# Kernel tuning notes

Measured on AMD Instinct MI355X. Metric: run time of the kernel, lower is better.

The kernel has to match this reference:

```python
import jax, jax.numpy as jnp
import numpy as np

B, N, D, H = 256, 128, 1024, 4096
PR = 0.2
K1 = int(D * (1 - PR))  # 819 channels kept before net1
K2 = int(H * (1 - PR))  # 3276 channels kept before net2


def setup_inputs() -> dict:
    key = jax.random.key(0)
    ks = jax.random.split(key, 5)
    s = 0.02
    return {
        "x": jax.random.normal(ks[0], (B, N, D), jnp.float32),
        "ws1": jax.random.normal(ks[1], (N,), jnp.float32) * s,  # get_scores1 weight [1,N] -> [N]
        "bs1": jnp.zeros((), jnp.float32),
        "W1": jax.random.normal(ks[2], (H, K1), jnp.float32) * s,  # net1 Linear(K1 -> H)
        "b1": jnp.zeros((H,), jnp.float32),
        "ws2": jax.random.normal(ks[3], (N,), jnp.float32) * s,  # get_scores2 weight
        "bs2": jnp.zeros((), jnp.float32),
        "W2": jax.random.normal(ks[4], (D, K2), jnp.float32) * s,  # net2 Linear(K2 -> D)
        "b2": jnp.zeros((D,), jnp.float32),
    }


def _prune(x, w_s, b_s, k):
    # x: [b, n, c]. Original scores each channel c with Linear(num_patches,1)
    # applied over the patch axis after rearrange to [b, c, n]; equivalent einsum here.
    scores = jnp.einsum('bnc,n->bc', x, w_s) + b_s            # [b, c]
    _, idx = jax.lax.top_k(scores, k)                          # top-k channels per sample
    idx = jnp.sort(idx, axis=-1)                               # boolean-mask gather preserves original channel order
    return jnp.take_along_axis(x, idx[:, None, :], axis=2)    # [b, n, k]


def reference(x, ws1, bs1, W1, b1, ws2, bs2, W2, b2):
    x1 = _prune(x, ws1, bs1, K1)                               # [b, n, K1]
    h = jax.nn.relu(jnp.einsum('bnk,hk->bnh', x1, W1) + b1)    # net1 (dropout=0 eval)
    h2 = _prune(h, ws2, bs2, K2)                               # [b, n, K2]
    return jnp.einsum('bnk,dk->bnd', h2, W2) + b2              # net2
```

## Files before the change

kernel.cpp:

```cpp
#include <hip/hip_runtime.h>
#include <cstdint>
#include <cstddef>

#define B_  256
#define N_  128
#define D_  1024
#define H_  4096
#define K1_ 819
#define K2_ 3276
#define K1P 832
#define K2P 3296
#define KT1 (K1P / 32)
#define KT2 (K2P / 32)

typedef __bf16 bf16x8 __attribute__((ext_vector_type(8)));
typedef float floatx4 __attribute__((ext_vector_type(4)));

__device__ __forceinline__ unsigned short f2bf(float f) {
  unsigned u = __float_as_uint(f);
  u += 0x7FFFu + ((u >> 16) & 1u);
  return (unsigned short)(u >> 16);
}
__device__ __forceinline__ float bf2f(unsigned short s) {
  return __uint_as_float(((unsigned)s) << 16);
}

#define GL16(gp, lp) __builtin_amdgcn_global_load_lds( \
    (const __attribute__((address_space(1))) void*)(gp), \
    (__attribute__((address_space(3))) void*)(lp), 16, 0, 0)

__global__ __launch_bounds__(256) void scores1_kernel(const float* __restrict__ x,
                                                      const float* __restrict__ ws1,
                                                      float* __restrict__ scores1) {
  int b = blockIdx.x, t = threadIdx.x;
  __shared__ float w[N_];
  if (t < N_) w[t] = ws1[t];
  __syncthreads();
  const float* xb = x + (size_t)b * N_ * D_;
  double a0 = 0, a1 = 0, a2 = 0, a3 = 0;
  for (int n = 0; n < N_; ++n) {
    double wv = (double)w[n];
    const float* r = xb + (size_t)n * D_ + t;
    a0 += (double)r[0]   * wv;
    a1 += (double)r[256] * wv;
    a2 += (double)r[512] * wv;
    a3 += (double)r[768] * wv;
  }
  float* s = scores1 + (size_t)b * D_ + t;
  s[0]   = (float)a0;
  s[256] = (float)a1;
  s[512] = (float)a2;
  s[768] = (float)a3;
}

__global__ __launch_bounds__(256) void topk_kernel(const float* __restrict__ scores,
                                                   int C, int K,
                                                   int* __restrict__ idx_out) {
  int b = blockIdx.x, t = threadIdx.x;
  __shared__ unsigned keys[4096];
  __shared__ unsigned hist[256];
  __shared__ unsigned sbuf[256];
  __shared__ unsigned s_sel, s_want, s_bgt, s_beq;

  for (int c = t; c < C; c += 256) {
    unsigned u = __float_as_uint(scores[(size_t)b * C + c]);
    keys[c] = u ^ ((u & 0x80000000u) ? 0xFFFFFFFFu : 0x80000000u);
  }
  if (t == 0) { s_want = (unsigned)K; s_bgt = 0u; s_beq = 0u; }
  __syncthreads();

  unsigned prefix = 0;
  for (int shift = 24; shift >= 0; shift -= 8) {
    hist[t] = 0u;
    __syncthreads();
    unsigned mask = (shift == 24) ? 0u : (0xFFFFFFFFu << (shift + 8));
    for (int c = t; c < C; c += 256) {
      unsigned k = keys[c];
      if ((k & mask) == (prefix & mask))
        atomicAdd(&hist[(k >> shift) & 0xFFu], 1u);
    }
    __syncthreads();
    if (t == 0) {
      unsigned want = s_want, cum = 0u, sel = 0u;
      for (int d = 255; d >= 0; --d) {
        cum += hist[d];
        if (cum >= want) { sel = (unsigned)d; s_want = want - (cum - hist[d]); break; }
      }
      s_sel = sel;
    }
    __syncthreads();
    prefix |= (s_sel << shift);
  }
  unsigned kth = prefix;
  unsigned n_eq_keep = s_want;
  __syncthreads();

  int nch = C >> 8;
  for (int ch = 0; ch < nch; ++ch) {
    int c = (ch << 8) + t;
    unsigned k = keys[c];
    unsigned gt = (k > kth) ? 1u : 0u;
    unsigned eq = (k == kth) ? 1u : 0u;
    unsigned val = gt | (eq << 16);
    sbuf[t] = val;
    __syncthreads();
    unsigned incl = val;
    for (int off = 1; off < 256; off <<= 1) {
      unsigned o = (t >= off) ? sbuf[t - off] : 0u;
      __syncthreads();
      incl += o;
      sbuf[t] = incl;
      __syncthreads();
    }
    unsigned excl = incl - val;
    unsigned gt_ex = excl & 0xFFFFu, eq_ex = excl >> 16;
    unsigned base_gt = s_bgt, base_eq = s_beq;
    unsigned eq_before = base_eq + eq_ex;
    bool keep = (gt != 0u) || ((eq != 0u) && (eq_before < n_eq_keep));
    unsigned kept_eq_before = (eq_before < n_eq_keep) ? eq_before : n_eq_keep;
    unsigned pos = base_gt + gt_ex + kept_eq_before;
    if (keep) idx_out[(size_t)b * K + pos] = c;
    __syncthreads();
    if (t == 255) {
      s_bgt = base_gt + (incl & 0xFFFFu);
      s_beq = base_eq + (incl >> 16);
    }
    __syncthreads();
  }
}

__global__ __launch_bounds__(256) void xprep_kernel(const float* __restrict__ x,
                                                    const int* __restrict__ idx1,
                                                    unsigned short* __restrict__ xch,
                                                    unsigned short* __restrict__ xcl) {
  int bn = blockIdx.x;
  int b = bn >> 7;
  const int* idxb = idx1 + (size_t)b * K1_;
  const float* xr = x + (size_t)bn * D_;
  unsigned short* oh = xch + (size_t)bn * K1P;
  unsigned short* ol = xcl + (size_t)bn * K1P;
  for (int j = threadIdx.x; j < K1P; j += 256) {
    float v = (j < K1_) ? xr[idxb[j]] : 0.f;
    unsigned short hi = f2bf(v);
    unsigned short lo = f2bf(v - bf2f(hi));
    oh[j] = hi;
    ol[j] = lo;
  }
}

__global__ __launch_bounds__(256) void w1split_kernel(const float* __restrict__ W1,
                                                      unsigned short* __restrict__ w1h,
                                                      unsigned short* __restrict__ w1l) {
  int e = blockIdx.x * 256 + threadIdx.x;
  int k = e % K1P, row = e / K1P;
  float v = (k < K1_) ? W1[(size_t)row * K1_ + k] : 0.f;
  unsigned short hi = f2bf(v);
  unsigned short lo = f2bf(v - bf2f(hi));
  w1h[e] = hi;
  w1l[e] = lo;
}

__global__ __launch_bounds__(256) void w2conv_kernel(const float* __restrict__ W2,
                                                     unsigned short* __restrict__ w2b) {
  int e = blockIdx.x * 256 + threadIdx.x;
  int k = e % K2P, row = e / K2P;
  w2b[e] = (k < K2_) ? f2bf(W2[(size_t)row * K2_ + k]) : (unsigned short)0;
}

__global__ __launch_bounds__(256) void hcompact_kernel(const unsigned short* __restrict__ h,
                                                       const int* __restrict__ idx2,
                                                       unsigned short* __restrict__ hcomp) {
  int bn = blockIdx.x;
  int b = bn >> 7;
  const int* idxb = idx2 + (size_t)b * K2_;
  const unsigned short* hr = h + (size_t)bn * H_;
  unsigned short* o = hcomp + (size_t)bn * K2P;
  for (int j = threadIdx.x; j < K2P; j += 256)
    o[j] = (j < K2_) ? hr[idxb[j]] : (unsigned short)0;
}

#define MF1(d, a, b) d = __builtin_amdgcn_mfma_f32_16x16x32_bf16(a, b, d, 0, 0, 0)

#define CLUSTER24(i0, A0H, A0L, A1H, A1L) \
  __builtin_amdgcn_s_setprio(1); \
  { _Pragma("unroll") \
    for (int j = 0; j < 4; ++j) { \
      MF1(acc[i0][j], A0H, bh[j]); \
      MF1(acc[i0][j], A0H, bl[j]); \
      MF1(acc[i0][j], A0L, bh[j]); \
      MF1(acc[(i0) + 1][j], A1H, bh[j]); \
      MF1(acc[(i0) + 1][j], A1H, bl[j]); \
      MF1(acc[(i0) + 1][j], A1L, bh[j]); \
    } } \
  __builtin_amdgcn_s_setprio(0);

__global__ __launch_bounds__(512, 2) void gemm1_kernel(
    const unsigned short* __restrict__ xch, const unsigned short* __restrict__ xcl,
    const unsigned short* __restrict__ w1h, const unsigned short* __restrict__ w1l,
    const float* __restrict__ b1, const float* __restrict__ ws2,
    unsigned short* __restrict__ h, float* __restrict__ scores2) {
  const int hc0 = blockIdx.x * 256;
  const int b0 = blockIdx.y * 2;
  const int t = threadIdx.x, w = t >> 6, lane = t & 63;
  const int ml = lane & 15, qd = lane >> 4;
  const int wm = w >> 2, wn = w & 3;

  __shared__ unsigned short Ah[2][8192], Al[2][8192], Bh[2][8192], Bl[2][8192];

  floatx4 acc[8][4] = {};

  const unsigned short* Abh = xch + (size_t)b0 * N_ * K1P;
  const unsigned short* Abl = xcl + (size_t)b0 * N_ * K1P;
  const unsigned short* Bbh = w1h + (size_t)hc0 * K1P;
  const unsigned short* Bbl = w1l + (size_t)hc0 * K1P;

  const int c0 = w * 64 + lane, c1 = c0 + 512;
  const size_t off0 = (size_t)(((c0 >> 6) << 4) | (c0 & 15)) * K1P + (size_t)(((c0 >> 4) & 3) * 8);
  const size_t off1 = (size_t)(((c1 >> 6) << 4) | (c1 & 15)) * K1P + (size_t)(((c1 >> 4) & 3) * 8);
  const int lb0 = (w * 64) * 8;
  const int lb1 = (512 + w * 64) * 8;

  auto aof = [&](int i) { return ((wm * 8 + i) * 64 + qd * 16 + ml) * 8; };

  GL16(Abh + off0, &Ah[0][lb0]); GL16(Abh + off1, &Ah[0][lb1]);
  GL16(Abl + off0, &Al[0][lb0]); GL16(Abl + off1, &Al[0][lb1]);
  GL16(Bbh + off0, &Bh[0][lb0]); GL16(Bbh + off1, &Bh[0][lb1]);
  GL16(Bbl + off0, &Bl[0][lb0]); GL16(Bbl + off1, &Bl[0][lb1]);

  for (int kt = 0; kt < KT1; ++kt) {
    const int cur = kt & 1, nxt = cur ^ 1;
    const size_t kk = (size_t)(kt + 1) * 32;
    const bool stg = (kt + 1 < KT1);

    if (stg) { GL16(Bbh + off0 + kk, &Bh[nxt][lb0]); GL16(Bbh + off1 + kk, &Bh[nxt][lb1]); }
    if (stg) asm volatile("s_waitcnt vmcnt(2)" ::: "memory");
    else     asm volatile("s_waitcnt vmcnt(0)" ::: "memory");
    __builtin_amdgcn_s_barrier();

    bf16x8 bh[4], bl[4];
#pragma unroll
    for (int j = 0; j < 4; ++j) {
      const int bo = ((wn * 4 + j) * 64 + qd * 16 + ml) * 8;
      bh[j] = *(const bf16x8*)&Bh[cur][bo];
      bl[j] = *(const bf16x8*)&Bl[cur][bo];
    }
    bf16x8 a0h = *(const bf16x8*)&Ah[cur][aof(0)];
    bf16x8 a0l = *(const bf16x8*)&Al[cur][aof(0)];
    bf16x8 a1h = *(const bf16x8*)&Ah[cur][aof(1)];
    bf16x8 a1l = *(const bf16x8*)&Al[cur][aof(1)];
    bf16x8 a2h = *(const bf16x8*)&Ah[cur][aof(2)];
    bf16x8 a2l = *(const bf16x8*)&Al[cur][aof(2)];
    bf16x8 a3h = *(const bf16x8*)&Ah[cur][aof(3)];
    bf16x8 a3l = *(const bf16x8*)&Al[cur][aof(3)];
    if (stg) { GL16(Bbl + off0 + kk, &Bl[nxt][lb0]); GL16(Bbl + off1 + kk, &Bl[nxt][lb1]); }
    __builtin_amdgcn_sched_barrier(0);
    CLUSTER24(0, a0h, a0l, a1h, a1l)
    __builtin_amdgcn_s_barrier();

    bf16x8 a4h = *(const bf16x8*)&Ah[cur][aof(4)];
    bf16x8 a4l = *(const bf16x8*)&Al[cur][aof(4)];
    bf16x8 a5h = *(const bf16x8*)&Ah[cur][aof(5)];
    bf16x8 a5l = *(const bf16x8*)&Al[cur][aof(5)];
    if (stg) { GL16(Abh + off0 + kk, &Ah[nxt][lb0]); GL16(Abh + off1 + kk, &Ah[nxt][lb1]); }
    __builtin_amdgcn_sched_barrier(0);
    CLUSTER24(2, a2h, a2l, a3h, a3l)
    __builtin_amdgcn_s_barrier();

    bf16x8 a6h = *(const bf16x8*)&Ah[cur][aof(6)];
    bf16x8 a6l = *(const bf16x8*)&Al[cur][aof(6)];
    bf16x8 a7h = *(const bf16x8*)&Ah[cur][aof(7)];
    bf16x8 a7l = *(const bf16x8*)&Al[cur][aof(7)];
    if (stg) { GL16(Abl + off0 + kk, &Al[nxt][lb0]); GL16(Abl + off1 + kk, &Al[nxt][lb1]); }
    __builtin_amdgcn_sched_barrier(0);
    CLUSTER24(4, a4h, a4l, a5h, a5l)
    __builtin_amdgcn_s_barrier();

    __builtin_amdgcn_sched_barrier(0);
    CLUSTER24(6, a6h, a6l, a7h, a7l)
    __builtin_amdgcn_s_barrier();
  }

  const int bb = b0 + wm;
  float bias[4];
#pragma unroll
  for (int j = 0; j < 4; ++j) bias[j] = b1[hc0 + wn * 64 + j * 16 + ml];
  float sc[4] = {0.f, 0.f, 0.f, 0.f};
#pragma unroll
  for (int i = 0; i < 8; ++i) {
#pragma unroll
    for (int r = 0; r < 4; ++r) {
      const int n = i * 16 + qd * 4 + r;
      const float wsn = ws2[n];
      unsigned short* hp = h + ((size_t)(bb * N_ + n)) * H_ + hc0 + wn * 64;
#pragma unroll
      for (int j = 0; j < 4; ++j) {
        float v = acc[i][j][r] + bias[j];
        v = fmaxf(v, 0.f);
        hp[j * 16 + ml] = f2bf(v);
        sc[j] += v * wsn;
      }
    }
  }
#pragma unroll
  for (int j = 0; j < 4; ++j) {
    sc[j] += __shfl_xor(sc[j], 16);
    sc[j] += __shfl_xor(sc[j], 32);
  }
  if (lane < 16) {
#pragma unroll
    for (int j = 0; j < 4; ++j)
      scores2[(size_t)bb * H_ + hc0 + wn * 64 + j * 16 + lane] = sc[j];
  }
}

#define MF2(d, a, b) d = __builtin_amdgcn_mfma_f32_16x16x32_bf16(a, b, d, 0, 0, 0)

#define CLUSTER8(i0, A0, A1) \
  __builtin_amdgcn_s_setprio(1); \
  { _Pragma("unroll") \
    for (int j = 0; j < 4; ++j) { \
      MF2(acc[i0][j], A0, bh[j]); \
      MF2(acc[(i0) + 1][j], A1, bh[j]); \
    } } \
  __builtin_amdgcn_s_setprio(0);

__global__ __launch_bounds__(512, 2) void gemm2_kernel(
    const unsigned short* __restrict__ hcomp, const unsigned short* __restrict__ w2b,
    const float* __restrict__ b2, float* __restrict__ out) {
  const int d0 = blockIdx.x * 256;
  const int b0 = blockIdx.y * 2;
  const int t = threadIdx.x, w = t >> 6, lane = t & 63;
  const int ml = lane & 15, qd = lane >> 4;
  const int wm = w >> 2, wn = w & 3;

  __shared__ unsigned short A2[2][8192], B2[2][8192];

  floatx4 acc[8][4] = {};

  const unsigned short* Ab = hcomp + (size_t)b0 * N_ * K2P;
  const unsigned short* Bb = w2b + (size_t)d0 * K2P;

  const int c0 = w * 64 + lane, c1 = c0 + 512;
  const size_t off0 = (size_t)(((c0 >> 6) << 4) | (c0 & 15)) * K2P + (size_t)(((c0 >> 4) & 3) * 8);
  const size_t off1 = (size_t)(((c1 >> 6) << 4) | (c1 & 15)) * K2P + (size_t)(((c1 >> 4) & 3) * 8);
  const int lb0 = (w * 64) * 8, lb1 = (512 + w * 64) * 8;

  auto aof = [&](int i) { return ((wm * 8 + i) * 64 + qd * 16 + ml) * 8; };

  GL16(Ab + off0, &A2[0][lb0]); GL16(Ab + off1, &A2[0][lb1]);
  GL16(Bb + off0, &B2[0][lb0]); GL16(Bb + off1, &B2[0][lb1]);

  for (int kt = 0; kt < KT2; ++kt) {
    const int cur = kt & 1, nxt = cur ^ 1;
    const size_t kk = (size_t)(kt + 1) * 32;
    const bool stg = (kt + 1 < KT2);

    if (stg) { GL16(Ab + off0 + kk, &A2[nxt][lb0]); GL16(Ab + off1 + kk, &A2[nxt][lb1]); }
    if (stg) asm volatile("s_waitcnt vmcnt(2)" ::: "memory");
    else     asm volatile("s_waitcnt vmcnt(0)" ::: "memory");
    __builtin_amdgcn_s_barrier();

    bf16x8 bh[4];
#pragma unroll
    for (int j = 0; j < 4; ++j) {
      const int bo = ((wn * 4 + j) * 64 + qd * 16 + ml) * 8;
      bh[j] = *(const bf16x8*)&B2[cur][bo];
    }
    bf16x8 a0 = *(const bf16x8*)&A2[cur][aof(0)];
    bf16x8 a1 = *(const bf16x8*)&A2[cur][aof(1)];
    bf16x8 a2 = *(const bf16x8*)&A2[cur][aof(2)];
    bf16x8 a3 = *(const bf16x8*)&A2[cur][aof(3)];
    if (stg) { GL16(Bb + off0 + kk, &B2[nxt][lb0]); GL16(Bb + off1 + kk, &B2[nxt][lb1]); }
    __builtin_amdgcn_sched_barrier(0);
    CLUSTER8(0, a0, a1)
    __builtin_amdgcn_s_barrier();

    bf16x8 a4 = *(const bf16x8*)&A2[cur][aof(4)];
    bf16x8 a5 = *(const bf16x8*)&A2[cur][aof(5)];
    __builtin_amdgcn_sched_barrier(0);
    CLUSTER8(2, a2, a3)
    __builtin_amdgcn_s_barrier();

    bf16x8 a6 = *(const bf16x8*)&A2[cur][aof(6)];
    bf16x8 a7 = *(const bf16x8*)&A2[cur][aof(7)];
    __builtin_amdgcn_sched_barrier(0);
    CLUSTER8(4, a4, a5)
    __builtin_amdgcn_s_barrier();

    __builtin_amdgcn_sched_barrier(0);
    CLUSTER8(6, a6, a7)
    __builtin_amdgcn_s_barrier();
  }

  const int bb = b0 + wm;
  float bias[4];
#pragma unroll
  for (int j = 0; j < 4; ++j) bias[j] = b2[d0 + wn * 64 + j * 16 + ml];
#pragma unroll
  for (int i = 0; i < 8; ++i) {
#pragma unroll
    for (int r = 0; r < 4; ++r) {
      const int n = i * 16 + qd * 4 + r;
      float* op = out + ((size_t)(bb * N_ + n)) * D_ + d0 + wn * 64;
#pragma unroll
      for (int j = 0; j < 4; ++j)
        op[j * 16 + ml] = acc[i][j][r] + bias[j];
    }
  }
}

extern "C" void kernel_launch(void* const* d_in, const int* in_sizes, int n_in,
                              void* d_out, int out_size, void* d_ws, size_t ws_size,
                              hipStream_t stream) {
  (void)in_sizes; (void)n_in; (void)out_size; (void)ws_size;
  const float* x   = (const float*)d_in[0];
  const float* ws1 = (const float*)d_in[1];
  const float* W1  = (const float*)d_in[3];
  const float* b1  = (const float*)d_in[4];
  const float* ws2 = (const float*)d_in[5];
  const float* W2  = (const float*)d_in[7];
  const float* b2  = (const float*)d_in[8];
  float* out = (float*)d_out;

  char* p = (char*)d_ws;
  auto alloc = [&](size_t bytes) {
    char* r = p;
    p += (bytes + 255) & ~(size_t)255;
    return r;
  };
  float* scores1 = (float*)alloc((size_t)B_ * D_ * sizeof(float));
  int*   idx1    = (int*)  alloc((size_t)B_ * K1_ * sizeof(int));
  float* scores2 = (float*)alloc((size_t)B_ * H_ * sizeof(float));
  int*   idx2    = (int*)  alloc((size_t)B_ * K2_ * sizeof(int));
  unsigned short* w1h = (unsigned short*)alloc((size_t)H_ * K1P * sizeof(short));
  unsigned short* w1l = (unsigned short*)alloc((size_t)H_ * K1P * sizeof(short));
  unsigned short* w2b = (unsigned short*)alloc((size_t)D_ * K2P * sizeof(short));
  unsigned short* h   = (unsigned short*)alloc((size_t)B_ * N_ * H_ * sizeof(short));
  size_t xc_bytes    = (size_t)B_ * N_ * K1P * sizeof(short);
  size_t hcomp_bytes = (size_t)B_ * N_ * K2P * sizeof(short);
  char* region = alloc(hcomp_bytes > 2 * xc_bytes ? hcomp_bytes : 2 * xc_bytes);
  unsigned short* xch   = (unsigned short*)region;
  unsigned short* xcl   = (unsigned short*)(region + xc_bytes);
  unsigned short* hcomp = (unsigned short*)region;

  scores1_kernel<<<B_, 256, 0, stream>>>(x, ws1, scores1);
  topk_kernel<<<B_, 256, 0, stream>>>(scores1, D_, K1_, idx1);
  xprep_kernel<<<B_ * N_, 256, 0, stream>>>(x, idx1, xch, xcl);
  w1split_kernel<<<(H_ * K1P) / 256, 256, 0, stream>>>(W1, w1h, w1l);
  w2conv_kernel<<<(D_ * K2P) / 256, 256, 0, stream>>>(W2, w2b);
  gemm1_kernel<<<dim3(H_ / 256, B_ / 2), 512, 0, stream>>>(xch, xcl, w1h, w1l, b1, ws2, h, scores2);
  topk_kernel<<<B_, 256, 0, stream>>>(scores2, H_, K2_, idx2);
  hcompact_kernel<<<B_ * N_, 256, 0, stream>>>(h, idx2, hcomp);
  gemm2_kernel<<<dim3(D_ / 256, B_ / 2), 512, 0, stream>>>(hcomp, w2b, b2, out);
}
```

Measured before the change: 1.650 ms.

## Deepen gemm2 K-step to 64, warp-shuffle top-k scan, vectorize gathers

gemm2 now handles 64 K elements per iteration in two 32-wide LDS halves, with K2P padded to 3328. Each A fragment is reused against four B fragments per cluster, and there are fewer loop-level waits and barriers. The top-k compaction scan swaps the 8-step shared-memory Hillis-Steele scan, which synchronises at every step, for wave shuffles plus a 4-entry cross-wave sum. xprep and hcompact now read indices as int4 and write 4-wide vectors, with index rows padded to LDI1/LDI2 so the vector loads stay aligned. The cost is double the LDS footprint in gemm2 and slightly more padding work in the K dimension.

```diff
diff --git a/kernel.cpp b/kernel.cpp
--- a/kernel.cpp
+++ b/kernel.cpp
@@ -9,12 +9,15 @@
 #define K1_ 819
 #define K2_ 3276
 #define K1P 832
-#define K2P 3296
+#define K2P 3328
 #define KT1 (K1P / 32)
-#define KT2 (K2P / 32)
+#define KT2D (K2P / 64)
+#define LDI1 820
+#define LDI2 3280
 
 typedef __bf16 bf16x8 __attribute__((ext_vector_type(8)));
 typedef float floatx4 __attribute__((ext_vector_type(4)));
+typedef unsigned short ushort4v __attribute__((ext_vector_type(4)));
 
 __device__ __forceinline__ unsigned short f2bf(float f) {
   unsigned u = __float_as_uint(f);
@@ -54,19 +57,20 @@
 }
 
 __global__ __launch_bounds__(256) void topk_kernel(const float* __restrict__ scores,
-                                                   int C, int K,
+                                                   int C, int K, int ldi,
                                                    int* __restrict__ idx_out) {
   int b = blockIdx.x, t = threadIdx.x;
+  const int lane = t & 63, wv = t >> 6;
   __shared__ unsigned keys[4096];
   __shared__ unsigned hist[256];
-  __shared__ unsigned sbuf[256];
-  __shared__ unsigned s_sel, s_want, s_bgt, s_beq;
+  __shared__ unsigned wsum[4];
+  __shared__ unsigned s_sel, s_want;
 
   for (int c = t; c < C; c += 256) {
     unsigned u = __float_as_uint(scores[(size_t)b * C + c]);
     keys[c] = u ^ ((u & 0x80000000u) ? 0xFFFFFFFFu : 0x80000000u);
   }
-  if (t == 0) { s_want = (unsigned)K; s_bgt = 0u; s_beq = 0u; }
+  if (t == 0) s_want = (unsigned)K;
   __syncthreads();
 
   unsigned prefix = 0;
@@ -95,6 +99,7 @@
   unsigned n_eq_keep = s_want;
   __syncthreads();
 
+  unsigned base_gt = 0u, base_eq = 0u;
   int nch = C >> 8;
   for (int ch = 0; ch < nch; ++ch) {
     int c = (ch << 8) + t;
@@ -102,29 +107,30 @@
     unsigned gt = (k > kth) ? 1u : 0u;
     unsigned eq = (k == kth) ? 1u : 0u;
     unsigned val = gt | (eq << 16);
-    sbuf[t] = val;
+    unsigned incl = val;
+#pragma unroll
+    for (int off = 1; off < 64; off <<= 1) {
+      unsigned o = __shfl_up(incl, off, 64);
+      if (lane >= off) incl += o;
+    }
+    if (lane == 63) wsum[wv] = incl;
     __syncthreads();
-    unsigned incl = val;
-    for (int off = 1; off < 256; off <<= 1) {
-      unsigned o = (t >= off) ? sbuf[t - off] : 0u;
-      __syncthreads();
-      incl += o;
-      sbuf[t] = incl;
-      __syncthreads();
-    }
-    unsigned excl = incl - val;
+    unsigned pre = 0u, tot = 0u;
+#pragma unroll
+    for (int u = 0; u < 4; ++u) {
+      unsigned s = wsum[u];
+      tot += s;
+      if (u < wv) pre += s;
+    }
+    unsigned excl = incl + pre - val;
     unsigned gt_ex = excl & 0xFFFFu, eq_ex = excl >> 16;
-    unsigned base_gt = s_bgt, base_eq = s_beq;
     unsigned eq_before = base_eq + eq_ex;
     bool keep = (gt != 0u) || ((eq != 0u) && (eq_before < n_eq_keep));
     unsigned kept_eq_before = (eq_before < n_eq_keep) ? eq_before : n_eq_keep;
     unsigned pos = base_gt + gt_ex + kept_eq_before;
-    if (keep) idx_out[(size_t)b * K + pos] = c;
-    __syncthreads();
-    if (t == 255) {
-      s_bgt = base_gt + (incl & 0xFFFFu);
-      s_beq = base_eq + (incl >> 16);
-    }
+    if (keep) idx_out[(size_t)b * ldi + pos] = c;
+    base_gt += tot & 0xFFFFu;
+    base_eq += tot >> 16;
     __syncthreads();
   }
 }
@@ -135,16 +141,31 @@
                                                     unsigned short* __restrict__ xcl) {
   int bn = blockIdx.x;
   int b = bn >> 7;
-  const int* idxb = idx1 + (size_t)b * K1_;
+  const int* idxb = idx1 + (size_t)b * LDI1;
   const float* xr = x + (size_t)bn * D_;
   unsigned short* oh = xch + (size_t)bn * K1P;
   unsigned short* ol = xcl + (size_t)bn * K1P;
-  for (int j = threadIdx.x; j < K1P; j += 256) {
-    float v = (j < K1_) ? xr[idxb[j]] : 0.f;
-    unsigned short hi = f2bf(v);
-    unsigned short lo = f2bf(v - bf2f(hi));
-    oh[j] = hi;
-    ol[j] = lo;
+  for (int j0 = threadIdx.x * 4; j0 < K1P; j0 += 1024) {
+    ushort4v vh, vl;
+    if (j0 + 3 < K1_) {
+      int4 id = *(const int4*)&idxb[j0];
+      float f0 = xr[id.x], f1 = xr[id.y], f2 = xr[id.z], f3 = xr[id.w];
+      vh[0] = f2bf(f0); vl[0] = f2bf(f0 - bf2f(vh[0]));
+      vh[1] = f2bf(f1); vl[1] = f2bf(f1 - bf2f(vh[1]));
+      vh[2] = f2bf(f2); vl[2] = f2bf(f2 - bf2f(vh[2]));
+      vh[3] = f2bf(f3); vl[3] = f2bf(f3 - bf2f(vh[3]));
+    } else {
+#pragma unroll
+      for (int e = 0; e < 4; ++e) {
+        int j = j0 + e;
+        float v = (j < K1_) ? xr[idxb[j]] : 0.f;
+        unsigned short hi = f2bf(v);
+        vh[e] = hi;
+        vl[e] = f2bf(v - bf2f(hi));
+      }
+    }
+    *(ushort4v*)&oh[j0] = vh;
+    *(ushort4v*)&ol[j0] = vl;
   }
 }
 
@@ -172,11 +193,19 @@
                                                        unsigned short* __restrict__ hcomp) {
   int bn = blockIdx.x;
   int b = bn >> 7;
-  const int* idxb = idx2 + (size_t)b * K2_;
+  const int* idxb = idx2 + (size_t)b * LDI2;
   const unsigned short* hr = h + (size_t)bn * H_;
   unsigned short* o = hcomp + (size_t)bn * K2P;
-  for (int j = threadIdx.x; j < K2P; j += 256)
-    o[j] = (j < K2_) ? hr[idxb[j]] : (unsigned short)0;
+  for (int j0 = threadIdx.x * 4; j0 < K2P; j0 += 1024) {
+    ushort4v v;
+    if (j0 < K2_) {
+      int4 id = *(const int4*)&idxb[j0];
+      v[0] = hr[id.x]; v[1] = hr[id.y]; v[2] = hr[id.z]; v[3] = hr[id.w];
+    } else {
+      v[0] = 0; v[1] = 0; v[2] = 0; v[3] = 0;
+    }
+    *(ushort4v*)&o[j0] = v;
+  }
 }
 
 #define MF1(d, a, b) d = __builtin_amdgcn_mfma_f32_16x16x32_bf16(a, b, d, 0, 0, 0)
@@ -315,12 +344,14 @@
 
 #define MF2(d, a, b) d = __builtin_amdgcn_mfma_f32_16x16x32_bf16(a, b, d, 0, 0, 0)
 
-#define CLUSTER8(i0, A0, A1) \
+#define CL16(i0, A0, A1, A2r, A3, BB) \
   __builtin_amdgcn_s_setprio(1); \
   { _Pragma("unroll") \
     for (int j = 0; j < 4; ++j) { \
-      MF2(acc[i0][j], A0, bh[j]); \
-      MF2(acc[(i0) + 1][j], A1, bh[j]); \
+      MF2(acc[(i0)][j], A0, BB[j]); \
+      MF2(acc[(i0) + 1][j], A1, BB[j]); \
+      MF2(acc[(i0) + 2][j], A2r, BB[j]); \
+      MF2(acc[(i0) + 3][j], A3, BB[j]); \
     } } \
   __builtin_amdgcn_s_setprio(0);
 
@@ -333,7 +364,7 @@
   const int ml = lane & 15, qd = lane >> 4;
   const int wm = w >> 2, wn = w & 3;
 
-  __shared__ unsigned short A2[2][8192], B2[2][8192];
+  __shared__ unsigned short As[2][2][8192], Bs[2][2][8192];
 
   floatx4 acc[8][4] = {};
 
@@ -346,49 +377,62 @@
   const int lb0 = (w * 64) * 8, lb1 = (512 + w * 64) * 8;
 
   auto aof = [&](int i) { return ((wm * 8 + i) * 64 + qd * 16 + ml) * 8; };
-
-  GL16(Ab + off0, &A2[0][lb0]); GL16(Ab + off1, &A2[0][lb1]);
-  GL16(Bb + off0, &B2[0][lb0]); GL16(Bb + off1, &B2[0][lb1]);
-
-  for (int kt = 0; kt < KT2; ++kt) {
+  auto bof = [&](int j) { return ((wn * 4 + j) * 64 + qd * 16 + ml) * 8; };
+
+  GL16(Ab + off0,      &As[0][0][lb0]); GL16(Ab + off1,      &As[0][0][lb1]);
+  GL16(Ab + off0 + 32, &As[0][1][lb0]); GL16(Ab + off1 + 32, &As[0][1][lb1]);
+  GL16(Bb + off0,      &Bs[0][0][lb0]); GL16(Bb + off1,      &Bs[0][0][lb1]);
+  GL16(Bb + off0 + 32, &Bs[0][1][lb0]); GL16(Bb + off1 + 32, &Bs[0][1][lb1]);
+
+  for (int kt = 0; kt < KT2D; ++kt) {
     const int cur = kt & 1, nxt = cur ^ 1;
-    const size_t kk = (size_t)(kt + 1) * 32;
-    const bool stg = (kt + 1 < KT2);
-
-    if (stg) { GL16(Ab + off0 + kk, &A2[nxt][lb0]); GL16(Ab + off1 + kk, &A2[nxt][lb1]); }
+    const size_t kk = (size_t)(kt + 1) * 64;
+    const bool stg = (kt + 1 < KT2D);
+
+    if (stg) { GL16(Ab + off0 + kk, &As[nxt][0][lb0]); GL16(Ab + off1 + kk, &As[nxt][0][lb1]); }
     if (stg) asm volatile("s_waitcnt vmcnt(2)" ::: "memory");
     else     asm volatile("s_waitcnt vmcnt(0)" ::: "memory");
     __builtin_amdgcn_s_barrier();
 
-    bf16x8 bh[4];
-#pragma unroll
-    for (int j = 0; j < 4; ++j) {
-      const int bo = ((wn * 4 + j) * 64 + qd * 16 + ml) * 8;
-      bh[j] = *(const bf16x8*)&B2[cur][bo];
-    }
-    bf16x8 a0 = *(const bf16x8*)&A2[cur][aof(0)];
-    bf16x8 a1 = *(const bf16x8*)&A2[cur][aof(1)];
-    bf16x8 a2 = *(const bf16x8*)&A2[cur][aof(2)];
-    bf16x8 a3 = *(const bf16x8*)&A2[cur][aof(3)];
-    if (stg) { GL16(Bb + off0 + kk, &B2[nxt][lb0]); GL16(Bb + off1 + kk, &B2[nxt][lb1]); }
-    __builtin_amdgcn_sched_barrier(0);
-    CLUSTER8(0, a0, a1)
-    __builtin_amdgcn_s_barrier();
-
-    bf16x8 a4 = *(const bf16x8*)&A2[cur][aof(4)];
-    bf16x8 a5 = *(const bf16x8*)&A2[cur][aof(5)];
-    __builtin_amdgcn_sched_barrier(0);
-    CLUSTER8(2, a2, a3)
-    __builtin_amdgcn_s_barrier();
-
-    bf16x8 a6 = *(const bf16x8*)&A2[cur][aof(6)];
-    bf16x8 a7 = *(const bf16x8*)&A2[cur][aof(7)];
-    __builtin_amdgcn_sched_barrier(0);
-    CLUSTER8(4, a4, a5)
-    __builtin_amdgcn_s_barrier();
-
-    __builtin_amdgcn_sched_barrier(0);
-    CLUSTER8(6, a6, a7)
+    bf16x8 bh0[4];
+#pragma unroll
+    for (int j = 0; j < 4; ++j) bh0[j] = *(const bf16x8*)&Bs[cur][0][bof(j)];
+    bf16x8 a0 = *(const bf16x8*)&As[cur][0][aof(0)];
+    bf16x8 a1 = *(const bf16x8*)&As[cur][0][aof(1)];
+    bf16x8 a2 = *(const bf16x8*)&As[cur][0][aof(2)];
+    bf16x8 a3 = *(const bf16x8*)&As[cur][0][aof(3)];
+    bf16x8 a4 = *(const bf16x8*)&As[cur][0][aof(4)];
+    bf16x8 a5 = *(const bf16x8*)&As[cur][0][aof(5)];
+    bf16x8 a6 = *(const bf16x8*)&As[cur][0][aof(6)];
+    bf16x8 a7 = *(const bf16x8*)&As[cur][0][aof(7)];
+    if (stg) { GL16(Ab + off0 + kk + 32, &As[nxt][1][lb0]); GL16(Ab + off1 + kk + 32, &As[nxt][1][lb1]); }
+    __builtin_amdgcn_sched_barrier(0);
+    CL16(0, a0, a1, a2, a3, bh0)
+    __builtin_amdgcn_s_barrier();
+
+    bf16x8 bh1[4];
+#pragma unroll
+    for (int j = 0; j < 4; ++j) bh1[j] = *(const bf16x8*)&Bs[cur][1][bof(j)];
+    bf16x8 e0 = *(const bf16x8*)&As[cur][1][aof(0)];
+    bf16x8 e1 = *(const bf16x8*)&As[cur][1][aof(1)];
+    bf16x8 e2 = *(const bf16x8*)&As[cur][1][aof(2)];
+    bf16x8 e3 = *(const bf16x8*)&As[cur][1][aof(3)];
+    if (stg) { GL16(Bb + off0 + kk, &Bs[nxt][0][lb0]); GL16(Bb + off1 + kk, &Bs[nxt][0][lb1]); }
+    __builtin_amdgcn_sched_barrier(0);
+    CL16(4, a4, a5, a6, a7, bh0)
+    __builtin_amdgcn_s_barrier();
+
+    bf16x8 e4 = *(const bf16x8*)&As[cur][1][aof(4)];
+    bf16x8 e5 = *(const bf16x8*)&As[cur][1][aof(5)];
+    bf16x8 e6 = *(const bf16x8*)&As[cur][1][aof(6)];
+    bf16x8 e7 = *(const bf16x8*)&As[cur][1][aof(7)];
+    if (stg) { GL16(Bb + off0 + kk + 32, &Bs[nxt][1][lb0]); GL16(Bb + off1 + kk + 32, &Bs[nxt][1][lb1]); }
+    __builtin_amdgcn_sched_barrier(0);
+    CL16(0, e0, e1, e2, e3, bh1)
+    __builtin_amdgcn_s_barrier();
+
+    __builtin_amdgcn_sched_barrier(0);
+    CL16(4, e4, e5, e6, e7, bh1)
     __builtin_amdgcn_s_barrier();
   }
 
@@ -429,9 +473,9 @@
     return r;
   };
   float* scores1 = (float*)alloc((size_t)B_ * D_ * sizeof(float));
-  int*   idx1    = (int*)  alloc((size_t)B_ * K1_ * sizeof(int));
+  int*   idx1    = (int*)  alloc((size_t)B_ * LDI1 * sizeof(int));
   float* scores2 = (float*)alloc((size_t)B_ * H_ * sizeof(float));
-  int*   idx2    = (int*)  alloc((size_t)B_ * K2_ * sizeof(int));
+  int*   idx2    = (int*)  alloc((size_t)B_ * LDI2 * sizeof(int));
   unsigned short* w1h = (unsigned short*)alloc((size_t)H_ * K1P * sizeof(short));
   unsigned short* w1l = (unsigned short*)alloc((size_t)H_ * K1P * sizeof(short));
   unsigned short* w2b = (unsigned short*)alloc((size_t)D_ * K2P * sizeof(short));
@@ -444,12 +488,12 @@
   unsigned short* hcomp = (unsigned short*)region;
 
   scores1_kernel<<<B_, 256, 0, stream>>>(x, ws1, scores1);
-  topk_kernel<<<B_, 256, 0, stream>>>(scores1, D_, K1_, idx1);
+  topk_kernel<<<B_, 256, 0, stream>>>(scores1, D_, K1_, LDI1, idx1);
   xprep_kernel<<<B_ * N_, 256, 0, stream>>>(x, idx1, xch, xcl);
   w1split_kernel<<<(H_ * K1P) / 256, 256, 0, stream>>>(W1, w1h, w1l);
   w2conv_kernel<<<(D_ * K2P) / 256, 256, 0, stream>>>(W2, w2b);
   gemm1_kernel<<<dim3(H_ / 256, B_ / 2), 512, 0, stream>>>(xch, xcl, w1h, w1l, b1, ws2, h, scores2);
-  topk_kernel<<<B_, 256, 0, stream>>>(scores2, H_, K2_, idx2);
+  topk_kernel<<<B_, 256, 0, stream>>>(scores2, H_, K2_, LDI2, idx2);
   hcompact_kernel<<<B_ * N_, 256, 0, stream>>>(h, idx2, hcomp);
   gemm2_kernel<<<dim3(D_ / 256, B_ / 2), 512, 0, stream>>>(hcomp, w2b, b2, out);
 }
```

Measured after the change: 1.437 ms. 1.15x faster.
